# Performance work log

Hardware: AMD Instinct MI355X
Metric: run time of the kernel (lower is better)

The kernel has to match this reference:

```python
import jax, jax.numpy as jnp
import numpy as np

HIDDEN = 2048
N_HEADS = 16
N_KV_HEADS = 4
HEAD_DIM = HIDDEN // N_HEADS  # 128
ROPE_DIM = 128
ROPE_BASE = 10000.0
B, T = 1, 2048


def rotate_half(x):
    x1 = x[..., ::2]
    x2 = x[..., 1::2]
    return jnp.concatenate([-x2, x1], axis=-1)


def setup_inputs() -> dict:
    key = jax.random.key(0)
    ks = jax.random.split(key, 6)
    x = jax.random.normal(ks[0], (B, T, HIDDEN), dtype=jnp.float32)
    # causal mask: True = masked out
    mask = jnp.triu(jnp.ones((T, T), dtype=bool), k=1)[None, None, :, :]
    s = 0.02
    Wq = jax.random.normal(ks[1], (HIDDEN, N_HEADS * HEAD_DIM), dtype=jnp.float32) * s
    Wk = jax.random.normal(ks[2], (HIDDEN, N_KV_HEADS * HEAD_DIM), dtype=jnp.float32) * s
    Wv = jax.random.normal(ks[3], (HIDDEN, N_KV_HEADS * HEAD_DIM), dtype=jnp.float32) * s
    Wo = jax.random.normal(ks[4], (N_HEADS * HEAD_DIM, HIDDEN), dtype=jnp.float32) * s
    rope_scale = jnp.ones((1,), dtype=jnp.float32)
    return {"x": x, "mask": mask, "Wq": Wq, "Wk": Wk, "Wv": Wv, "Wo": Wo,
            "rope_scale": rope_scale, "pos_offset": 0}


def reference(x, mask, Wq, Wk, Wv, Wo, rope_scale, pos_offset):
    Bb, Tt, C = x.shape
    # projections -> [B, H, T, D]
    q = (x @ Wq).reshape(Bb, Tt, N_HEADS, HEAD_DIM).transpose(0, 2, 1, 3)
    k = (x @ Wk).reshape(Bb, Tt, N_KV_HEADS, HEAD_DIM).transpose(0, 2, 1, 3)
    v = (x @ Wv).reshape(Bb, Tt, N_KV_HEADS, HEAD_DIM).transpose(0, 2, 1, 3)
    # GQA expansion (repeat_interleave over head dim)
    rep = N_HEADS // N_KV_HEADS
    k = jnp.repeat(k, rep, axis=1)
    v = jnp.repeat(v, rep, axis=1)
    # RoPE on first rope_dim dims
    rd = min(ROPE_DIM, HEAD_DIM)
    pos = jnp.arange(pos_offset, pos_offset + Tt, dtype=jnp.float32)
    inv_freq = 1.0 / (ROPE_BASE ** (jnp.arange(0, rd, 2, dtype=jnp.float32) / rd))
    freqs = jnp.einsum('i,j->ij', pos, inv_freq)          # [T, rd/2]
    emb = jnp.concatenate([freqs, freqs], axis=-1) * rope_scale  # [T, rd]
    cos = jnp.cos(emb)[None, None, :, :]
    sin = jnp.sin(emb)[None, None, :, :]
    q1, q2 = q[..., :rd], q[..., rd:]
    k1, k2 = k[..., :rd], k[..., rd:]
    q1 = q1 * cos + rotate_half(q1) * sin
    k1 = k1 * cos + rotate_half(k1) * sin
    q = jnp.concatenate([q1, q2], axis=-1)
    k = jnp.concatenate([k1, k2], axis=-1)
    # attention
    scale = HEAD_DIM ** -0.5
    scores = jnp.einsum('bhqd,bhkd->bhqk', q, k) * scale
    neg = jnp.finfo(scores.dtype).min
    scores = jnp.where(mask, neg, scores)
    probs = jax.nn.softmax(scores, axis=-1)
    out = jnp.einsum('bhqk,bhkd->bhqd', probs, v)
    out = out.transpose(0, 2, 1, 3).reshape(Bb, Tt, N_HEADS * HEAD_DIM)
    return out @ Wo
```

## Files before the change

kernel.cpp:

```cpp
#include <hip/hip_runtime.h>

typedef unsigned short u16;
typedef unsigned int u32;
typedef __attribute__((ext_vector_type(8))) short bf16x8;
typedef __attribute__((ext_vector_type(4))) float f32x4;
typedef __attribute__((ext_vector_type(4))) unsigned short u16x4;

#define MFMA16(a,b,c) __builtin_amdgcn_mfma_f32_16x16x32_bf16((a),(b),(c),0,0,0)

__device__ __forceinline__ u16 f2b(float f){
  union { float f; u32 u; } x; x.f = f;
  u32 r = x.u + 0x7fffu + ((x.u >> 16) & 1u);
  return (u16)(r >> 16);
}
__device__ __forceinline__ float b2f(u16 u){
  union { u32 u; float f; } x; x.u = ((u32)u) << 16; return x.f;
}

__global__ void cvt_bf16(const float* __restrict__ in, u16* __restrict__ out, int n4){
  int i = blockIdx.x * blockDim.x + threadIdx.x;
  int stride = gridDim.x * blockDim.x;
  for (; i < n4; i += stride){
    f32x4 v = ((const f32x4*)in)[i];
    u16x4 o = { f2b(v.x), f2b(v.y), f2b(v.z), f2b(v.w) };
    ((u16x4*)out)[i] = o;
  }
}

__global__ void transpose_cvt(const float* __restrict__ in, u16* __restrict__ out,
                              int inLd, int outLd){
  __shared__ __align__(16) float tile[64][68];
  int n0 = blockIdx.x * 64, k0 = blockIdx.y * 64;
  int t = threadIdx.x;
  int r = t & 63, cg = t >> 6;
  for (int j = 0; j < 4; ++j){
    int c = cg * 4 + j * 16;
    f32x4 v = *(const f32x4*)&in[(size_t)(k0 + r) * inLd + n0 + c];
    *(f32x4*)&tile[r][c] = v;
  }
  __syncthreads();
  for (int j = 0; j < 4; ++j){
    int c = cg * 4 + j * 16;
    u16x4 o = { f2b(tile[c+0][r]), f2b(tile[c+1][r]), f2b(tile[c+2][r]), f2b(tile[c+3][r]) };
    *(u16x4*)&out[(size_t)(n0 + r) * outLd + k0 + c] = o;
  }
}

__global__ void transpose_v(const u16* __restrict__ qkv, u16* __restrict__ vt){
  __shared__ __align__(16) u16 tile[64][72];
  int t0 = blockIdx.x * 64, d0 = blockIdx.y * 64, kh = blockIdx.z;
  int tt = threadIdx.x;
  int r = tt & 63, cg = tt >> 6;
  for (int j = 0; j < 2; ++j){
    int c = cg * 8 + j * 32;
    *(bf16x8*)&tile[r][c] = *(const bf16x8*)&qkv[(size_t)(t0 + r) * 3072 + 2560 + kh*128 + d0 + c];
  }
  __syncthreads();
  for (int j = 0; j < 2; ++j){
    int c = cg * 8 + j * 32;
    bf16x8 o = { (short)tile[c+0][r], (short)tile[c+1][r], (short)tile[c+2][r], (short)tile[c+3][r],
                 (short)tile[c+4][r], (short)tile[c+5][r], (short)tile[c+6][r], (short)tile[c+7][r] };
    *(bf16x8*)&vt[(size_t)(kh*128 + d0 + r) * 2048 + t0 + c] = o;
  }
}

template<bool BF16OUT>
__global__ __launch_bounds__(256) void gemm_bt(const u16* __restrict__ A, const u16* __restrict__ Bt,
                                               void* __restrict__ Cv, int M, int N, int K){
  __shared__ __align__(16) u16 Alds[128*64];
  __shared__ __align__(16) u16 Blds[128*64];
  int m0 = blockIdx.y * 128, n0 = blockIdx.x * 128;
  int t = threadIdx.x;
  int lane = t & 63, wid = t >> 6;
  int wr = wid >> 1, wc = wid & 1;
  int r16 = lane & 15, g = lane >> 4;
  f32x4 acc[4][4] = {};
  int off = (wid * 4) * 512 + lane * 8;
  for (int kb = 0; kb < K; kb += 64){
    #pragma unroll
    for (int i = 0; i < 4; ++i){
      int o = off + i * 512;
      int row = o >> 6, col = o & 63;
      __builtin_amdgcn_global_load_lds(
        (const __attribute__((address_space(1))) void*)&A[(size_t)(m0 + row) * K + kb + col],
        (__attribute__((address_space(3))) void*)&Alds[(wid*4 + i) * 512], 16, 0, 0);
    }
    #pragma unroll
    for (int i = 0; i < 4; ++i){
      int o = off + i * 512;
      int row = o >> 6, col = o & 63;
      __builtin_amdgcn_global_load_lds(
        (const __attribute__((address_space(1))) void*)&Bt[(size_t)(n0 + row) * K + kb + col],
        (__attribute__((address_space(3))) void*)&Blds[(wid*4 + i) * 512], 16, 0, 0);
    }
    __syncthreads();
    #pragma unroll
    for (int kc = 0; kc < 2; ++kc){
      bf16x8 af[4], bfr[4];
      #pragma unroll
      for (int mi = 0; mi < 4; ++mi)
        af[mi] = *(const bf16x8*)&Alds[(wr*64 + mi*16 + r16) * 64 + kc*32 + g*8];
      #pragma unroll
      for (int ni = 0; ni < 4; ++ni)
        bfr[ni] = *(const bf16x8*)&Blds[(wc*64 + ni*16 + r16) * 64 + kc*32 + g*8];
      #pragma unroll
      for (int mi = 0; mi < 4; ++mi)
        #pragma unroll
        for (int ni = 0; ni < 4; ++ni)
          acc[mi][ni] = MFMA16(af[mi], bfr[ni], acc[mi][ni]);
    }
    __syncthreads();
  }
  #pragma unroll
  for (int mi = 0; mi < 4; ++mi)
    #pragma unroll
    for (int ni = 0; ni < 4; ++ni){
      int row0 = m0 + wr*64 + mi*16 + g*4;
      int col  = n0 + wc*64 + ni*16 + r16;
      #pragma unroll
      for (int r = 0; r < 4; ++r){
        float v = acc[mi][ni][r];
        if (BF16OUT) ((u16*)Cv)[(size_t)(row0 + r) * N + col] = f2b(v);
        else         ((float*)Cv)[(size_t)(row0 + r) * N + col] = v;
      }
    }
}

__global__ void rope_kernel(const u16* __restrict__ qkv, u16* __restrict__ qb, u16* __restrict__ kb,
                            const float* __restrict__ rsp, const int* __restrict__ pop){
  int t = blockIdx.x;
  const u16* row = qkv + (size_t)t * 3072;
  float rs = rsp[0];
  int p = pop[0] + t;
  for (int idx = threadIdx.x; idx < 2560; idx += blockDim.x){
    int h = idx >> 7, d = idx & 127;
    const u16* hp = row + (h << 7);
    int e = d & 63;
    double invf = exp((double)e * -0.14391156381125648);
    double ang = (double)p * invf * (double)rs;
    ang = fmod(ang, 6.283185307179586476925286766559);
    float fa = (float)ang;
    float ca = cosf(fa), sa = sinf(fa);
    float v;
    if (d < 64) v = b2f(hp[d]) * ca - b2f(hp[2*d+1]) * sa;
    else        v = b2f(hp[d]) * ca + b2f(hp[2*e]) * sa;
    u16 o = f2b(v);
    if (h < 16) qb[((size_t)(h*2048 + t))*128 + d] = o;
    else        kb[((size_t)((h-16)*2048 + t))*128 + d] = o;
  }
}

__global__ __launch_bounds__(256, 1) void attn_kernel(const u16* __restrict__ qb, const u16* __restrict__ kb,
                                                      const u16* __restrict__ vt, u16* __restrict__ attn2){
  __shared__ __align__(16) u16 P4[4][2][16][40];
  int h = blockIdx.y, kh = h >> 2;
  int t = threadIdx.x, lane = t & 63, wid = t >> 6;
  int r16 = lane & 15, g = lane >> 4;
  int wt = blockIdx.x * 4 + wid;
  int pairi = wt >> 1;
  int qt32 = (wt & 1) ? (63 - pairi) : pairi;
  int qbase = qt32 * 32;
  int nt = qt32 + 1;

  bf16x8 qf0[4], qf1[4];
  const u16* q0p = qb + ((size_t)(h*2048 + qbase + r16)) * 128;
  #pragma unroll
  for (int dc = 0; dc < 4; ++dc){
    qf0[dc] = *(const bf16x8*)&q0p[dc*32 + g*8];
    qf1[dc] = *(const bf16x8*)&q0p[16*128 + dc*32 + g*8];
  }

  const u16* kbase = kb + (size_t)kh * 2048 * 128;
  const u16* vbase = vt + (size_t)kh * 128 * 2048;

  float l0 = 0.f, l1 = 0.f;
  f32x4 acc0[8] = {}, acc1[8] = {};
  const float scale = 0.08838834764831845f;

  auto LOADK = [&](bf16x8 (&kr)[8], int tile){
    const u16* kp = kbase + (size_t)(tile*32 + r16) * 128;
    #pragma unroll
    for (int dc = 0; dc < 4; ++dc){
      kr[dc]     = *(const bf16x8*)&kp[dc*32 + g*8];
      kr[4 + dc] = *(const bf16x8*)&kp[16*128 + dc*32 + g*8];
    }
  };

  auto COMPUTE = [&](bf16x8 (&kr)[8], int tile){
    bf16x8 vr[8];
    int kcol = tile*32 + g*8;
    #pragma unroll
    for (int dt = 0; dt < 8; ++dt)
      vr[dt] = *(const bf16x8*)&vbase[(size_t)(dt*16 + r16) * 2048 + kcol];
    f32x4 sA0 = {0.f,0.f,0.f,0.f}, sA1 = {0.f,0.f,0.f,0.f};
    f32x4 sB0 = {0.f,0.f,0.f,0.f}, sB1 = {0.f,0.f,0.f,0.f};
    #pragma unroll
    for (int dc = 0; dc < 4; ++dc){
      sA0 = MFMA16(kr[dc],   qf0[dc], sA0);
      sA1 = MFMA16(kr[dc],   qf1[dc], sA1);
      sB0 = MFMA16(kr[4+dc], qf0[dc], sB0);
      sB1 = MFMA16(kr[4+dc], qf1[dc], sB1);
    }
    float x0[8], x1[8];
    #pragma unroll
    for (int r = 0; r < 4; ++r){
      x0[r] = sA0[r] * scale; x0[4+r] = sB0[r] * scale;
      x1[r] = sA1[r] * scale; x1[4+r] = sB1[r] * scale;
    }
    if (tile == qt32){
      int q0r = qbase + r16, q1r = q0r + 16;
      #pragma unroll
      for (int hf = 0; hf < 2; ++hf)
        #pragma unroll
        for (int r = 0; r < 4; ++r){
          int k = tile*32 + hf*16 + g*4 + r;
          if (k > q0r) x0[hf*4 + r] = -1e30f;
          if (k > q1r) x1[hf*4 + r] = -1e30f;
        }
    }
    float ps0 = 0.f, ps1 = 0.f;
    #pragma unroll
    for (int j = 0; j < 8; ++j){
      x0[j] = __expf(x0[j]); ps0 += x0[j];
      x1[j] = __expf(x1[j]); ps1 += x1[j];
    }
    l0 += ps0; l1 += ps1;
    u16x4 a0 = { f2b(x0[0]), f2b(x0[1]), f2b(x0[2]), f2b(x0[3]) };
    u16x4 b0 = { f2b(x0[4]), f2b(x0[5]), f2b(x0[6]), f2b(x0[7]) };
    u16x4 a1 = { f2b(x1[0]), f2b(x1[1]), f2b(x1[2]), f2b(x1[3]) };
    u16x4 b1 = { f2b(x1[4]), f2b(x1[5]), f2b(x1[6]), f2b(x1[7]) };
    *(u16x4*)&P4[wid][0][r16][g*4]      = a0;
    *(u16x4*)&P4[wid][0][r16][16+g*4]   = b0;
    *(u16x4*)&P4[wid][1][r16][g*4]      = a1;
    *(u16x4*)&P4[wid][1][r16][16+g*4]   = b1;
    asm volatile("s_waitcnt lgkmcnt(0)" ::: "memory");
    bf16x8 pa0 = *(const bf16x8*)&P4[wid][0][r16][g*8];
    bf16x8 pa1 = *(const bf16x8*)&P4[wid][1][r16][g*8];
    #pragma unroll
    for (int dt = 0; dt < 8; ++dt){
      acc0[dt] = MFMA16(pa0, vr[dt], acc0[dt]);
      acc1[dt] = MFMA16(pa1, vr[dt], acc1[dt]);
    }
  };

  bf16x8 kA[8], kB[8];
  LOADK(kA, 0);
  int it = 0;
  while (true){
    if (it + 1 < nt) LOADK(kB, it + 1);
    COMPUTE(kA, it);
    ++it; if (it >= nt) break;
    if (it + 1 < nt) LOADK(kA, it + 1);
    COMPUTE(kB, it);
    ++it; if (it >= nt) break;
  }

  l0 += __shfl_xor(l0, 16); l0 += __shfl_xor(l0, 32);
  l1 += __shfl_xor(l1, 16); l1 += __shfl_xor(l1, 32);
  float rq0[4], rq1[4];
  #pragma unroll
  for (int r = 0; r < 4; ++r){
    rq0[r] = 1.f / __shfl(l0, g*4 + r);
    rq1[r] = 1.f / __shfl(l1, g*4 + r);
  }
  #pragma unroll
  for (int dt = 0; dt < 8; ++dt)
    #pragma unroll
    for (int r = 0; r < 4; ++r){
      attn2[(size_t)(qbase + g*4 + r)      * 2048 + h*128 + dt*16 + r16] = f2b(acc0[dt][r] * rq0[r]);
      attn2[(size_t)(qbase + 16 + g*4 + r) * 2048 + h*128 + dt*16 + r16] = f2b(acc1[dt][r] * rq1[r]);
    }
}

extern "C" void kernel_launch(void* const* d_in, const int* in_sizes, int n_in,
                              void* d_out, int out_size, void* d_ws, size_t ws_size,
                              hipStream_t stream) {
  const float* x   = (const float*)d_in[0];
  const float* Wq  = (const float*)d_in[2];
  const float* Wk  = (const float*)d_in[3];
  const float* Wv  = (const float*)d_in[4];
  const float* Wo  = (const float*)d_in[5];
  const float* rs  = (const float*)d_in[6];
  const int*   po  = (const int*)d_in[7];
  float* out = (float*)d_out;

  u16* ws    = (u16*)d_ws;
  u16* xb    = ws;
  u16* wqkv  = xb   + 4194304;
  u16* wo_t  = wqkv + 6291456;
  u16* qkv   = wo_t + 4194304;
  u16* qb    = qkv  + 6291456;
  u16* kb2   = qb   + 4194304;
  u16* vt    = kb2  + 1048576;
  u16* attn2 = vt   + 1048576;

  cvt_bf16<<<2048, 256, 0, stream>>>(x, xb, 1048576);
  transpose_cvt<<<dim3(32,32), 256, 0, stream>>>(Wq, wqkv,             2048, 2048);
  transpose_cvt<<<dim3(8, 32), 256, 0, stream>>>(Wk, wqkv + 2048*2048, 512,  2048);
  transpose_cvt<<<dim3(8, 32), 256, 0, stream>>>(Wv, wqkv + 2560*2048, 512,  2048);
  transpose_cvt<<<dim3(32,32), 256, 0, stream>>>(Wo, wo_t,             2048, 2048);

  gemm_bt<true><<<dim3(24,16), 256, 0, stream>>>(xb, wqkv, qkv, 2048, 3072, 2048);
  rope_kernel<<<2048, 256, 0, stream>>>(qkv, qb, kb2, rs, po);
  transpose_v<<<dim3(32,2,4), 256, 0, stream>>>(qkv, vt);
  attn_kernel<<<dim3(16,16), 256, 0, stream>>>(qb, kb2, vt, attn2);
  gemm_bt<false><<<dim3(16,16), 256, 0, stream>>>(attn2, wo_t, out, 2048, 2048, 2048);
}
```

Measured before the change: 324.2 us.

## Split attention KV tiles across warps with LDS reduction and precompute RoPE table

The attention kernel now assigns one 32-row query tile per block. Its four waves each take every fourth KV tile and their partial accumulators and row sums are combined through a two-stage shared-memory reduction. The grid grows from 16x16 to 64x16 blocks and launch bounds allow two blocks per CU, giving more parallelism and better balance across the causal triangle. Separately, RoPE cos/sin values are built once into a table held in the now-unused bf16 x buffer, instead of computing double-precision exp/fmod/sincos per element. The reduction adds LDS traffic and barriers, and the doubled occupancy target may pressure registers.

After: 364.5 us. +12.4%, slower.

```diff
diff --git a/kernel.cpp b/kernel.cpp
--- a/kernel.cpp
+++ b/kernel.cpp
@@ -126,41 +126,45 @@
     }
 }
 
+__global__ void build_rope_tab(const float* __restrict__ rsp, const int* __restrict__ pop,
+                               float2* __restrict__ tab){
+  int i = blockIdx.x * blockDim.x + threadIdx.x;
+  int t = i >> 6, e = i & 63;
+  int p = pop[0] + t;
+  double invf = exp((double)e * -0.14391156381125648);
+  double ang = fmod((double)p * invf * (double)rsp[0], 6.283185307179586476925286766559);
+  float fa = (float)ang;
+  tab[i] = make_float2(cosf(fa), sinf(fa));
+}
+
 __global__ void rope_kernel(const u16* __restrict__ qkv, u16* __restrict__ qb, u16* __restrict__ kb,
-                            const float* __restrict__ rsp, const int* __restrict__ pop){
+                            const float2* __restrict__ tab){
   int t = blockIdx.x;
   const u16* row = qkv + (size_t)t * 3072;
-  float rs = rsp[0];
-  int p = pop[0] + t;
+  const float2* trow = tab + t * 64;
   for (int idx = threadIdx.x; idx < 2560; idx += blockDim.x){
     int h = idx >> 7, d = idx & 127;
     const u16* hp = row + (h << 7);
     int e = d & 63;
-    double invf = exp((double)e * -0.14391156381125648);
-    double ang = (double)p * invf * (double)rs;
-    ang = fmod(ang, 6.283185307179586476925286766559);
-    float fa = (float)ang;
-    float ca = cosf(fa), sa = sinf(fa);
+    float2 cs = trow[e];
     float v;
-    if (d < 64) v = b2f(hp[d]) * ca - b2f(hp[2*d+1]) * sa;
-    else        v = b2f(hp[d]) * ca + b2f(hp[2*e]) * sa;
+    if (d < 64) v = b2f(hp[d]) * cs.x - b2f(hp[2*d+1]) * cs.y;
+    else        v = b2f(hp[d]) * cs.x + b2f(hp[2*e]) * cs.y;
     u16 o = f2b(v);
     if (h < 16) qb[((size_t)(h*2048 + t))*128 + d] = o;
     else        kb[((size_t)((h-16)*2048 + t))*128 + d] = o;
   }
 }
 
-__global__ __launch_bounds__(256, 1) void attn_kernel(const u16* __restrict__ qb, const u16* __restrict__ kb,
+__global__ __launch_bounds__(256, 2) void attn_kernel(const u16* __restrict__ qb, const u16* __restrict__ kb,
                                                       const u16* __restrict__ vt, u16* __restrict__ attn2){
   __shared__ __align__(16) u16 P4[4][2][16][40];
+  __shared__ float red[2][64][66];
   int h = blockIdx.y, kh = h >> 2;
   int t = threadIdx.x, lane = t & 63, wid = t >> 6;
   int r16 = lane & 15, g = lane >> 4;
-  int wt = blockIdx.x * 4 + wid;
-  int pairi = wt >> 1;
-  int qt32 = (wt & 1) ? (63 - pairi) : pairi;
+  int qt32 = 63 - blockIdx.x;
   int qbase = qt32 * 32;
-  int nt = qt32 + 1;
 
   bf16x8 qf0[4], qf1[4];
   const u16* q0p = qb + ((size_t)(h*2048 + qbase + r16)) * 128;
@@ -243,33 +247,78 @@
     }
   };
 
+  int nj = (wid <= qt32) ? ((qt32 - wid) >> 2) + 1 : 0;
   bf16x8 kA[8], kB[8];
-  LOADK(kA, 0);
-  int it = 0;
-  while (true){
-    if (it + 1 < nt) LOADK(kB, it + 1);
-    COMPUTE(kA, it);
-    ++it; if (it >= nt) break;
-    if (it + 1 < nt) LOADK(kA, it + 1);
-    COMPUTE(kB, it);
-    ++it; if (it >= nt) break;
-  }
-
-  l0 += __shfl_xor(l0, 16); l0 += __shfl_xor(l0, 32);
-  l1 += __shfl_xor(l1, 16); l1 += __shfl_xor(l1, 32);
-  float rq0[4], rq1[4];
-  #pragma unroll
-  for (int r = 0; r < 4; ++r){
-    rq0[r] = 1.f / __shfl(l0, g*4 + r);
-    rq1[r] = 1.f / __shfl(l1, g*4 + r);
-  }
-  #pragma unroll
-  for (int dt = 0; dt < 8; ++dt)
+  if (nj > 0) LOADK(kA, wid);
+  int j = 0;
+  while (j < nj){
+    if (j + 1 < nj) LOADK(kB, wid + 4*(j+1));
+    COMPUTE(kA, wid + 4*j);
+    ++j; if (j >= nj) break;
+    if (j + 1 < nj) LOADK(kA, wid + 4*(j+1));
+    COMPUTE(kB, wid + 4*j);
+    ++j;
+  }
+
+  if (wid >= 2){
+    int s = wid - 2;
+    #pragma unroll
+    for (int dt = 0; dt < 8; ++dt)
+      #pragma unroll
+      for (int r = 0; r < 4; ++r){
+        red[s][lane][dt*4 + r]      = acc0[dt][r];
+        red[s][lane][32 + dt*4 + r] = acc1[dt][r];
+      }
+    red[s][lane][64] = l0; red[s][lane][65] = l1;
+  }
+  __syncthreads();
+  if (wid < 2){
+    #pragma unroll
+    for (int dt = 0; dt < 8; ++dt)
+      #pragma unroll
+      for (int r = 0; r < 4; ++r){
+        acc0[dt][r] += red[wid][lane][dt*4 + r];
+        acc1[dt][r] += red[wid][lane][32 + dt*4 + r];
+      }
+    l0 += red[wid][lane][64]; l1 += red[wid][lane][65];
+  }
+  __syncthreads();
+  if (wid == 1){
+    #pragma unroll
+    for (int dt = 0; dt < 8; ++dt)
+      #pragma unroll
+      for (int r = 0; r < 4; ++r){
+        red[0][lane][dt*4 + r]      = acc0[dt][r];
+        red[0][lane][32 + dt*4 + r] = acc1[dt][r];
+      }
+    red[0][lane][64] = l0; red[0][lane][65] = l1;
+  }
+  __syncthreads();
+  if (wid == 0){
+    #pragma unroll
+    for (int dt = 0; dt < 8; ++dt)
+      #pragma unroll
+      for (int r = 0; r < 4; ++r){
+        acc0[dt][r] += red[0][lane][dt*4 + r];
+        acc1[dt][r] += red[0][lane][32 + dt*4 + r];
+      }
+    l0 += red[0][lane][64]; l1 += red[0][lane][65];
+    l0 += __shfl_xor(l0, 16); l0 += __shfl_xor(l0, 32);
+    l1 += __shfl_xor(l1, 16); l1 += __shfl_xor(l1, 32);
+    float rq0[4], rq1[4];
     #pragma unroll
     for (int r = 0; r < 4; ++r){
-      attn2[(size_t)(qbase + g*4 + r)      * 2048 + h*128 + dt*16 + r16] = f2b(acc0[dt][r] * rq0[r]);
-      attn2[(size_t)(qbase + 16 + g*4 + r) * 2048 + h*128 + dt*16 + r16] = f2b(acc1[dt][r] * rq1[r]);
-    }
+      rq0[r] = 1.f / __shfl(l0, g*4 + r);
+      rq1[r] = 1.f / __shfl(l1, g*4 + r);
+    }
+    #pragma unroll
+    for (int dt = 0; dt < 8; ++dt)
+      #pragma unroll
+      for (int r = 0; r < 4; ++r){
+        attn2[(size_t)(qbase + g*4 + r)      * 2048 + h*128 + dt*16 + r16] = f2b(acc0[dt][r] * rq0[r]);
+        attn2[(size_t)(qbase + 16 + g*4 + r) * 2048 + h*128 + dt*16 + r16] = f2b(acc1[dt][r] * rq1[r]);
+      }
+  }
 }
 
 extern "C" void kernel_launch(void* const* d_in, const int* in_sizes, int n_in,
@@ -293,6 +342,7 @@
   u16* kb2   = qb   + 4194304;
   u16* vt    = kb2  + 1048576;
   u16* attn2 = vt   + 1048576;
+  float2* tab = (float2*)xb;
 
   cvt_bf16<<<2048, 256, 0, stream>>>(x, xb, 1048576);
   transpose_cvt<<<dim3(32,32), 256, 0, stream>>>(Wq, wqkv,             2048, 2048);
@@ -301,8 +351,9 @@
   transpose_cvt<<<dim3(32,32), 256, 0, stream>>>(Wo, wo_t,             2048, 2048);
 
   gemm_bt<true><<<dim3(24,16), 256, 0, stream>>>(xb, wqkv, qkv, 2048, 3072, 2048);
-  rope_kernel<<<2048, 256, 0, stream>>>(qkv, qb, kb2, rs, po);
+  build_rope_tab<<<512, 256, 0, stream>>>(rs, po, tab);
+  rope_kernel<<<2048, 256, 0, stream>>>(qkv, qb, kb2, tab);
   transpose_v<<<dim3(32,2,4), 256, 0, stream>>>(qkv, vt);
-  attn_kernel<<<dim3(16,16), 256, 0, stream>>>(qb, kb2, vt, attn2);
+  attn_kernel<<<dim3(64,16), 256, 0, stream>>>(qb, kb2, vt, attn2);
   gemm_bt<false><<<dim3(16,16), 256, 0, stream>>>(attn2, wo_t, out, 2048, 2048, 2048);
 }
```
